# Kernel optimization log

Measured on AMD Instinct MI355X. Metric: run time of the kernel, lower is better.

Reference implementation:

```python
import jax, jax.numpy as jnp
import numpy as np

ROI = 268          # nodes per graph / input feature dim
G = 512            # graphs in batch
N = G * ROI        # total nodes = 137216
E = 1000000        # total edges
CH = 32            # GIN hidden channels
SLOPE = 0.33       # leaky relu negative slope
BN_EPS = 1e-5


def _leaky(h):
    return jnp.where(h > 0, h, SLOPE * h)


def _bn(h, g, b, m, v):
    # inference-mode batch norm with running stats
    return (h - m) * jax.lax.rsqrt(v + BN_EPS) * g + b


def _gin(x, src, dst, eps, W1, b1, W2, b2, g, b, m, v):
    # GINConv: mlp((1+eps)*x + sum_{j->i} x_j), then BN + LeakyReLU
    agg = jax.ops.segment_sum(x[src], dst, num_segments=x.shape[0])
    h = (1.0 + eps) * x + agg
    h = _leaky(h @ W1 + b1) @ W2 + b2
    return _leaky(_bn(h, g, b, m, v))


def _pool(x, batch, counts):
    mx = jax.ops.segment_max(x, batch, num_segments=G)
    mn = jax.ops.segment_sum(x, batch, num_segments=G) / counts[:, None]
    return jnp.concatenate([mx, mn], axis=-1)


def setup_inputs() -> dict:
    key = jax.random.key(0)
    ks = jax.random.split(key, 16)
    x = jax.random.normal(ks[0], (N, ROI), dtype=jnp.float32)
    # edges constrained within each graph: node = graph_id*ROI + local_idx
    gid = jax.random.randint(ks[1], (E,), 0, G, dtype=jnp.int32)
    src = gid * ROI + jax.random.randint(ks[2], (E,), 0, ROI, dtype=jnp.int32)
    dst = gid * ROI + jax.random.randint(ks[3], (E,), 0, ROI, dtype=jnp.int32)
    edge_index = jnp.stack([src, dst], axis=0)
    batch = jnp.repeat(jnp.arange(G, dtype=jnp.int32), ROI)

    def lin(k, fi, fo):
        return jax.random.normal(k, (fi, fo), dtype=jnp.float32) / np.sqrt(fi)

    kp = jax.random.split(ks[4], 16)
    inp = {
        'x': x, 'edge_index': edge_index, 'batch': batch,
        # GIN layer 0 (268 -> 32)
        'eps0': jnp.zeros((), jnp.float32),
        'W1_0': lin(kp[0], ROI, CH), 'b1_0': jnp.zeros((CH,), jnp.float32),
        'W2_0': lin(kp[1], CH, CH), 'b2_0': jnp.zeros((CH,), jnp.float32),
        'bn0_g': jnp.ones((CH,), jnp.float32), 'bn0_b': jnp.zeros((CH,), jnp.float32),
        'bn0_m': jnp.zeros((CH,), jnp.float32), 'bn0_v': jnp.ones((CH,), jnp.float32),
        # GIN layer 1 (32 -> 32)
        'eps1': jnp.zeros((), jnp.float32),
        'W1_1': lin(kp[2], CH, CH), 'b1_1': jnp.zeros((CH,), jnp.float32),
        'W2_1': lin(kp[3], CH, CH), 'b2_1': jnp.zeros((CH,), jnp.float32),
        'bn1_g': jnp.ones((CH,), jnp.float32), 'bn1_b': jnp.zeros((CH,), jnp.float32),
        'bn1_m': jnp.zeros((CH,), jnp.float32), 'bn1_v': jnp.ones((CH,), jnp.float32),
        # readout head: 4*CH=128 -> 256 -> 128 -> 1
        'lin1_W': lin(kp[4], 4 * CH, 256), 'lin1_b': jnp.zeros((256,), jnp.float32),
        'hbn1_g': jnp.ones((256,), jnp.float32), 'hbn1_b': jnp.zeros((256,), jnp.float32),
        'hbn1_m': jnp.zeros((256,), jnp.float32), 'hbn1_v': jnp.ones((256,), jnp.float32),
        'lin2_W': lin(kp[5], 256, 128), 'lin2_b': jnp.zeros((128,), jnp.float32),
        'hbn2_g': jnp.ones((128,), jnp.float32), 'hbn2_b': jnp.zeros((128,), jnp.float32),
        'hbn2_m': jnp.zeros((128,), jnp.float32), 'hbn2_v': jnp.ones((128,), jnp.float32),
        'lin3_W': lin(kp[6], 128, 1), 'lin3_b': jnp.zeros((1,), jnp.float32),
    }
    return inp


def reference(x, edge_index, batch,
              eps0, W1_0, b1_0, W2_0, b2_0, bn0_g, bn0_b, bn0_m, bn0_v,
              eps1, W1_1, b1_1, W2_1, b2_1, bn1_g, bn1_b, bn1_m, bn1_v,
              lin1_W, lin1_b, hbn1_g, hbn1_b, hbn1_m, hbn1_v,
              lin2_W, lin2_b, hbn2_g, hbn2_b, hbn2_m, hbn2_v,
              lin3_W, lin3_b):
    src, dst = edge_index[0], edge_index[1]
    counts = jax.ops.segment_sum(jnp.ones((x.shape[0],), x.dtype), batch, num_segments=G)
    h0 = _gin(x, src, dst, eps0, W1_0, b1_0, W2_0, b2_0, bn0_g, bn0_b, bn0_m, bn0_v)
    p0 = _pool(h0, batch, counts)                      # [G, 2*CH]
    h1 = _gin(h0, src, dst, eps1, W1_1, b1_1, W2_1, b2_1, bn1_g, bn1_b, bn1_m, bn1_v)
    p1 = _pool(h1, batch, counts)                      # [G, 2*CH]
    z = jnp.concatenate([p0, p1], axis=-1)             # [G, 4*CH]
    z = _leaky(_bn(z @ lin1_W + lin1_b, hbn1_g, hbn1_b, hbn1_m, hbn1_v))
    z = _leaky(_bn(z @ lin2_W + lin2_b, hbn2_g, hbn2_b, hbn2_m, hbn2_v))
    return z @ lin3_W + lin3_b                          # [G, 1]
```

## Files before the change

kernel.cpp:

```cpp
#include <hip/hip_runtime.h>

#define ROI 268
#define NG 512
#define NNODES (NG * ROI)
#define CH 32
#define SLOPE 0.33f
#define BN_EPS 1e-5f
#define SR 34
#define SAS 258
#define RPS (ROI + 1)

__device__ __forceinline__ float leakyf(float v) {
    return v > 0.f ? v : SLOPE * v;
}

__global__ __launch_bounds__(256)
__attribute__((amdgpu_waves_per_eu(2, 4))) void k_gemm1(
    const float* __restrict__ x, const float* __restrict__ W1,
    float* __restrict__ y0) {
    __shared__ float sW[ROI * CH];
    __shared__ float sA[32 * SAS];

    const int tid = threadIdx.x;
    const int l = tid & 63;
    const int wcb = __builtin_amdgcn_readfirstlane((tid >> 6) << 3);
    const size_t rowbase = (size_t)blockIdx.x * 256;

    float acc[4][8];
#pragma unroll
    for (int r = 0; r < 4; r++)
#pragma unroll
        for (int c = 0; c < 8; c++) acc[r][c] = 0.f;

#pragma unroll
    for (int i = 0; i < 9; i++) {
        int f = (i << 8) + tid;
        if (f < (ROI * CH) / 4) ((float4*)sW)[f] = ((const float4*)W1)[f];
    }

    float4 pf[8];
#pragma unroll
    for (int i = 0; i < 8; i++) {
        int f = (i << 8) + tid;
        int row = f >> 3, kc = (f & 7) << 2;
        pf[i] = *(const float4*)&x[(rowbase + row) * ROI + kc];
    }

    int k0 = 0;
    for (int chunk = 0; chunk < 9; ++chunk) {
        const int ksize = (chunk < 8) ? 32 : 12;
        if (ksize == 32) {
#pragma unroll
            for (int i = 0; i < 8; i++) {
                int f = (i << 8) + tid;
                int row = f >> 3, kc = (f & 7) << 2;
                sA[(kc + 0) * SAS + row] = pf[i].x;
                sA[(kc + 1) * SAS + row] = pf[i].y;
                sA[(kc + 2) * SAS + row] = pf[i].z;
                sA[(kc + 3) * SAS + row] = pf[i].w;
            }
        } else {
#pragma unroll
            for (int i = 0; i < 3; i++) {
                int kc = i << 2;
                sA[(kc + 0) * SAS + tid] = pf[i].x;
                sA[(kc + 1) * SAS + tid] = pf[i].y;
                sA[(kc + 2) * SAS + tid] = pf[i].z;
                sA[(kc + 3) * SAS + tid] = pf[i].w;
            }
        }
        __syncthreads();
        if (chunk + 1 < 9) {
            const int nk0 = k0 + ksize;
            if (chunk + 1 < 8) {
#pragma unroll
                for (int i = 0; i < 8; i++) {
                    int f = (i << 8) + tid;
                    int row = f >> 3, kc = (f & 7) << 2;
                    pf[i] = *(const float4*)&x[(rowbase + row) * ROI + nk0 + kc];
                }
            } else {
#pragma unroll
                for (int i = 0; i < 3; i++)
                    pf[i] = *(const float4*)&x[(rowbase + tid) * ROI + nk0 + (i << 2)];
            }
        }
        const float* wp = &sW[k0 * CH + wcb];
#pragma unroll 2
        for (int kk = 0; kk < ksize; ++kk) {
            float2 a0 = *(const float2*)&sA[kk * SAS + 2 * l];
            float2 a1 = *(const float2*)&sA[kk * SAS + 128 + 2 * l];
            float4 w0 = *(const float4*)&wp[kk * CH];
            float4 w1 = *(const float4*)&wp[kk * CH + 4];
            float av[4] = {a0.x, a0.y, a1.x, a1.y};
            float wv[8] = {w0.x, w0.y, w0.z, w0.w, w1.x, w1.y, w1.z, w1.w};
#pragma unroll
            for (int r = 0; r < 4; r++)
#pragma unroll
                for (int c = 0; c < 8; c++) acc[r][c] += av[r] * wv[c];
        }
        k0 += ksize;
        __syncthreads();
    }

#pragma unroll
    for (int r = 0; r < 4; r++) {
        size_t row = rowbase + ((r < 2) ? (2 * l + r) : (126 + 2 * l + r));
        *(float4*)&y0[row * CH + wcb] =
            make_float4(acc[r][0], acc[r][1], acc[r][2], acc[r][3]);
        *(float4*)&y0[row * CH + wcb + 4] =
            make_float4(acc[r][4], acc[r][5], acc[r][6], acc[r][7]);
    }
}

__global__ void k_deg(const int* __restrict__ dst, int E, int* __restrict__ deg) {
    int stride = gridDim.x * blockDim.x;
    for (int i = blockIdx.x * blockDim.x + threadIdx.x; i < E; i += stride)
        atomicAdd(&deg[dst[i]], 1);
}

__global__ __launch_bounds__(512) void k_scan_local(
    int* __restrict__ deg, int* __restrict__ ticket, int* __restrict__ row_ptr) {
    __shared__ int s[512];
    __shared__ int sbase;
    const int g = blockIdx.x, t = threadIdx.x;
    int v = (t < ROI) ? deg[g * ROI + t] : 0;
    s[t] = v;
    __syncthreads();
    for (int d = 1; d < 512; d <<= 1) {
        int u = (t >= d) ? s[t - d] : 0;
        __syncthreads();
        s[t] += u;
        __syncthreads();
    }
    if (t == 511) sbase = atomicAdd(ticket, s[511]);
    __syncthreads();
    const int base = sbase;
    if (t < ROI) {
        int exc = base + s[t] - v;
        row_ptr[g * RPS + t] = exc;
        deg[g * ROI + t] = exc;
    }
    if (t == 511) row_ptr[g * RPS + ROI] = base + s[511];
}

__global__ void k_fill(const int* __restrict__ src, const int* __restrict__ dst,
                       int E, int* __restrict__ rcur, int* __restrict__ ebuf) {
    int stride = gridDim.x * blockDim.x;
    for (int i = blockIdx.x * blockDim.x + threadIdx.x; i < E; i += stride) {
        int d = dst[i];
        int g = d / ROI;
        int pos = atomicAdd(&rcur[d], 1);
        ebuf[pos] = (src[i] - g * ROI) * SR;
    }
}

__device__ __forceinline__ void gather_combine(
    const float* __restrict__ in, float* __restrict__ out,
    const int* __restrict__ rp, const int* __restrict__ ebuf, float e,
    const float* __restrict__ b1, int t) {
    const int ch = t & 31;
    const int hw = t >> 5;
    for (int n = hw; n < ROI; n += 16) {
        int b = rp[n], en = rp[n + 1];
        float acc = 0.f;
        int j = b;
        for (; j + 3 < en; j += 4) {
            int p0 = ebuf[j], p1 = ebuf[j + 1], p2 = ebuf[j + 2], p3 = ebuf[j + 3];
            float v0 = in[p0 + ch], v1 = in[p1 + ch];
            float v2 = in[p2 + ch], v3 = in[p3 + ch];
            acc += (v0 + v1) + (v2 + v3);
        }
        for (; j < en; ++j) acc += in[ebuf[j] + ch];
        out[n * SR + ch] = leakyf(e * in[n * SR + ch] + acc + b1[ch]);
    }
}

template <bool AFFINE>
__device__ __forceinline__ void gemm_inplace(float* __restrict__ buf,
                                             const float* __restrict__ w,
                                             const float* __restrict__ bias,
                                             const float* __restrict__ sc,
                                             const float* __restrict__ sh, int t) {
    for (int u = t; u < ROI * 2; u += 512) {
        const int r0 = (u >> 2) * 2;
        const int cq = u & 3;
        float acc0[8], acc1[8];
#pragma unroll
        for (int c = 0; c < 8; c++) {
            float b = AFFINE ? bias[cq * 8 + c] : 0.f;
            acc0[c] = b;
            acc1[c] = b;
        }
        const float* row0 = &buf[r0 * SR];
        const float* row1 = row0 + SR;
#pragma unroll 2
        for (int k = 0; k < CH; k += 2) {
            float2 a0 = *(const float2*)&row0[k];
            float2 a1 = *(const float2*)&row1[k];
            const float* wr0 = &w[k * CH + cq * 8];
            const float* wr1 = wr0 + CH;
            float4 wa = *(const float4*)wr0;
            float4 wb = *(const float4*)(wr0 + 4);
            float4 wc = *(const float4*)wr1;
            float4 wd = *(const float4*)(wr1 + 4);
            acc0[0] += a0.x * wa.x + a0.y * wc.x;
            acc0[1] += a0.x * wa.y + a0.y * wc.y;
            acc0[2] += a0.x * wa.z + a0.y * wc.z;
            acc0[3] += a0.x * wa.w + a0.y * wc.w;
            acc0[4] += a0.x * wb.x + a0.y * wd.x;
            acc0[5] += a0.x * wb.y + a0.y * wd.y;
            acc0[6] += a0.x * wb.z + a0.y * wd.z;
            acc0[7] += a0.x * wb.w + a0.y * wd.w;
            acc1[0] += a1.x * wa.x + a1.y * wc.x;
            acc1[1] += a1.x * wa.y + a1.y * wc.y;
            acc1[2] += a1.x * wa.z + a1.y * wc.z;
            acc1[3] += a1.x * wa.w + a1.y * wc.w;
            acc1[4] += a1.x * wb.x + a1.y * wd.x;
            acc1[5] += a1.x * wb.y + a1.y * wd.y;
            acc1[6] += a1.x * wb.z + a1.y * wd.z;
            acc1[7] += a1.x * wb.w + a1.y * wd.w;
        }
        float* o0 = &buf[r0 * SR + cq * 8];
        float* o1 = o0 + SR;
#pragma unroll
        for (int c = 0; c < 8; c += 2) {
            float h00 = acc0[c], h01 = acc0[c + 1];
            float h10 = acc1[c], h11 = acc1[c + 1];
            if (AFFINE) {
                float s0 = sc[cq * 8 + c], t0 = sh[cq * 8 + c];
                float s1 = sc[cq * 8 + c + 1], t1 = sh[cq * 8 + c + 1];
                h00 = leakyf(h00 * s0 + t0);
                h01 = leakyf(h01 * s1 + t1);
                h10 = leakyf(h10 * s0 + t0);
                h11 = leakyf(h11 * s1 + t1);
            }
            *(float2*)&o0[c] = make_float2(h00, h01);
            *(float2*)&o1[c] = make_float2(h10, h11);
        }
    }
}

__device__ __forceinline__ void pool_store(const float* __restrict__ h,
                                           float* __restrict__ psc, int t) {
    const int ch = t & 31;
    const int hw = t >> 5;
    const int wave = t >> 6;
    float s = 0.f, m = -1e30f;
    for (int n = hw; n < ROI; n += 16) {
        float v = h[n * SR + ch];
        s += v;
        m = fmaxf(m, v);
    }
    s += __shfl_down(s, 32);
    m = fmaxf(m, __shfl_down(m, 32));
    if ((t & 63) < 32) {
        psc[wave * 32 + ch] = s;
        psc[256 + wave * 32 + ch] = m;
    }
}

__device__ __forceinline__ void pool_final(const float* __restrict__ psc,
                                           float* __restrict__ zg, int t) {
    if (t < 32) {
        float s = 0.f, m = -1e30f;
#pragma unroll
        for (int wv = 0; wv < 8; wv++) {
            s += psc[wv * 32 + t];
            m = fmaxf(m, psc[256 + wv * 32 + t]);
        }
        zg[t] = m;
        zg[CH + t] = s / (float)ROI;
    }
}

__global__ __launch_bounds__(512, 2) void k_gin(
    const float* __restrict__ y0, const int* __restrict__ row_ptr,
    const int* __restrict__ ebuf, const float* __restrict__ eps0p,
    const float* __restrict__ b1_0, const float* __restrict__ W2_0,
    const float* __restrict__ b2_0, const float* __restrict__ bn0_g,
    const float* __restrict__ bn0_b, const float* __restrict__ bn0_m,
    const float* __restrict__ bn0_v, const float* __restrict__ eps1p,
    const float* __restrict__ W1_1, const float* __restrict__ b1_1,
    const float* __restrict__ W2_1, const float* __restrict__ b2_1,
    const float* __restrict__ bn1_g, const float* __restrict__ bn1_b,
    const float* __restrict__ bn1_m, const float* __restrict__ bn1_v,
    float* __restrict__ z) {
    __shared__ float bufA[ROI * SR];
    __shared__ float bufB[ROI * SR];
    __shared__ float w[CH * CH];
    __shared__ float prm[8 * CH];
    __shared__ float psc[512];
    __shared__ float epss[2];

    const int t = threadIdx.x;
    const int g = blockIdx.x;

    if (t < CH) {
        prm[0 * CH + t] = b1_0[t];
        prm[1 * CH + t] = b2_0[t];
        float s0 = bn0_g[t] * rsqrtf(bn0_v[t] + BN_EPS);
        prm[2 * CH + t] = s0;
        prm[3 * CH + t] = bn0_b[t] - bn0_m[t] * s0;
        prm[4 * CH + t] = b1_1[t];
        prm[5 * CH + t] = b2_1[t];
        float s1 = bn1_g[t] * rsqrtf(bn1_v[t] + BN_EPS);
        prm[6 * CH + t] = s1;
        prm[7 * CH + t] = bn1_b[t] - bn1_m[t] * s1;
    }
    if (t == 0) {
        epss[0] = 1.0f + *eps0p;
        epss[1] = 1.0f + *eps1p;
    }

    const float* yg = y0 + (size_t)g * ROI * CH;
    for (int f = t; f < (ROI * CH) / 4; f += 512) {
        float4 v = ((const float4*)yg)[f];
        int row = f >> 3, c4 = (f & 7) << 2;
        float* p = &bufA[row * SR + c4];
        *(float2*)p = make_float2(v.x, v.y);
        *(float2*)(p + 2) = make_float2(v.z, v.w);
    }
    for (int i = t; i < (CH * CH) / 4; i += 512)
        ((float4*)w)[i] = ((const float4*)W2_0)[i];
    __syncthreads();

    const int* rp = row_ptr + g * RPS;

    gather_combine(bufA, bufB, rp, ebuf, epss[0], &prm[0 * CH], t);
    __syncthreads();

    gemm_inplace<true>(bufB, w, &prm[1 * CH], &prm[2 * CH], &prm[3 * CH], t);
    __syncthreads();

    pool_store(bufB, psc, t);
    for (int i = t; i < (CH * CH) / 4; i += 512)
        ((float4*)w)[i] = ((const float4*)W1_1)[i];
    __syncthreads();

    pool_final(psc, z + (size_t)g * 128, t);
    gemm_inplace<false>(bufB, w, nullptr, nullptr, nullptr, t);
    __syncthreads();

    gather_combine(bufB, bufA, rp, ebuf, epss[1], &prm[4 * CH], t);
    for (int i = t; i < (CH * CH) / 4; i += 512)
        ((float4*)w)[i] = ((const float4*)W2_1)[i];
    __syncthreads();

    gemm_inplace<true>(bufA, w, &prm[5 * CH], &prm[6 * CH], &prm[7 * CH], t);
    __syncthreads();

    pool_store(bufA, psc, t);
    __syncthreads();
    pool_final(psc, z + (size_t)g * 128 + 64, t);
}

__global__ __launch_bounds__(256) void k_head(
    const float* __restrict__ z, const float* __restrict__ W1,
    const float* __restrict__ b1, const float* __restrict__ g1,
    const float* __restrict__ be1, const float* __restrict__ m1,
    const float* __restrict__ v1, const float* __restrict__ W2,
    const float* __restrict__ b2, const float* __restrict__ g2,
    const float* __restrict__ be2, const float* __restrict__ m2,
    const float* __restrict__ v2, const float* __restrict__ W3,
    const float* __restrict__ b3, float* __restrict__ out) {
    __shared__ float zr[128], z1[256], z2[128];
    const int t = threadIdx.x;
    const int g = blockIdx.x;

    if (t < 32) ((float4*)zr)[t] = ((const float4*)(z + (size_t)g * 128))[t];
    __syncthreads();
    {
        float acc = b1[t];
#pragma unroll 8
        for (int k = 0; k < 128; k++) acc += zr[k] * W1[k * 256 + t];
        float s = g1[t] * rsqrtf(v1[t] + BN_EPS);
        acc = (acc - m1[t]) * s + be1[t];
        z1[t] = leakyf(acc);
    }
    __syncthreads();
    if (t < 128) {
        float acc = b2[t];
#pragma unroll 8
        for (int k = 0; k < 256; k++) acc += z1[k] * W2[k * 128 + t];
        float s = g2[t] * rsqrtf(v2[t] + BN_EPS);
        acc = (acc - m2[t]) * s + be2[t];
        z2[t] = leakyf(acc);
    }
    __syncthreads();
    if (t < 64) {
        float v = z2[t] * W3[t] + z2[t + 64] * W3[t + 64];
        for (int offd = 32; offd; offd >>= 1) v += __shfl_down(v, offd);
        if (t == 0) out[g] = v + b3[0];
    }
}

extern "C" void kernel_launch(void* const* d_in, const int* in_sizes, int n_in,
                              void* d_out, int out_size, void* d_ws, size_t ws_size,
                              hipStream_t stream) {
    const float* x      = (const float*)d_in[0];
    const int* eidx     = (const int*)d_in[1];
    const float* eps0   = (const float*)d_in[3];
    const float* W1_0   = (const float*)d_in[4];
    const float* b1_0   = (const float*)d_in[5];
    const float* W2_0   = (const float*)d_in[6];
    const float* b2_0   = (const float*)d_in[7];
    const float* bn0_g  = (const float*)d_in[8];
    const float* bn0_b  = (const float*)d_in[9];
    const float* bn0_m  = (const float*)d_in[10];
    const float* bn0_v  = (const float*)d_in[11];
    const float* eps1   = (const float*)d_in[12];
    const float* W1_1   = (const float*)d_in[13];
    const float* b1_1   = (const float*)d_in[14];
    const float* W2_1   = (const float*)d_in[15];
    const float* b2_1   = (const float*)d_in[16];
    const float* bn1_g  = (const float*)d_in[17];
    const float* bn1_b  = (const float*)d_in[18];
    const float* bn1_m  = (const float*)d_in[19];
    const float* bn1_v  = (const float*)d_in[20];
    const float* lin1_W = (const float*)d_in[21];
    const float* lin1_b = (const float*)d_in[22];
    const float* hbn1_g = (const float*)d_in[23];
    const float* hbn1_b = (const float*)d_in[24];
    const float* hbn1_m = (const float*)d_in[25];
    const float* hbn1_v = (const float*)d_in[26];
    const float* lin2_W = (const float*)d_in[27];
    const float* lin2_b = (const float*)d_in[28];
    const float* hbn2_g = (const float*)d_in[29];
    const float* hbn2_b = (const float*)d_in[30];
    const float* hbn2_m = (const float*)d_in[31];
    const float* hbn2_v = (const float*)d_in[32];
    const float* lin3_W = (const float*)d_in[33];
    const float* lin3_b = (const float*)d_in[34];

    const int E = in_sizes[1] / 2;
    const int* src = eidx;
    const int* dst = eidx + E;

    char* ws = (char*)d_ws;
    const size_t Y0_OFF  = 0;
    const size_t Z_OFF   = (size_t)NNODES * CH * 4;
    const size_t DEG_OFF = Z_OFF + (size_t)NG * 128 * 4;
    const size_t TKT_OFF = DEG_OFF + (size_t)NNODES * 4;
    const size_t RP_OFF  = TKT_OFF + 64;
    const size_t EB_OFF  = RP_OFF + (size_t)(NG * RPS + 4) * 4;

    float* y0    = (float*)(ws + Y0_OFF);
    float* z     = (float*)(ws + Z_OFF);
    int* deg     = (int*)(ws + DEG_OFF);
    int* ticket  = (int*)(ws + TKT_OFF);
    int* row_ptr = (int*)(ws + RP_OFF);
    int* ebuf    = (int*)(ws + EB_OFF);

    k_gemm1<<<NNODES / 256, 256, 0, stream>>>(x, W1_0, y0);

    hipMemsetAsync(deg, 0, (size_t)NNODES * sizeof(int) + 64, stream);
    k_deg<<<1024, 256, 0, stream>>>(dst, E, deg);
    k_scan_local<<<NG, 512, 0, stream>>>(deg, ticket, row_ptr);
    k_fill<<<1024, 256, 0, stream>>>(src, dst, E, deg, ebuf);

    k_gin<<<NG, 512, 0, stream>>>(y0, row_ptr, ebuf, eps0, b1_0, W2_0, b2_0,
                                  bn0_g, bn0_b, bn0_m, bn0_v, eps1, W1_1, b1_1,
                                  W2_1, b2_1, bn1_g, bn1_b, bn1_m, bn1_v, z);

    k_head<<<NG, 256, 0, stream>>>(z, lin1_W, lin1_b, hbn1_g, hbn1_b, hbn1_m,
                                   hbn1_v, lin2_W, lin2_b, hbn2_g, hbn2_b,
                                   hbn2_m, hbn2_v, lin3_W, lin3_b,
                                   (float*)d_out);
}
```

Measured before the change: 507.6 us.

## Replace LDS-tiled first-layer GEMM with one-row-per-thread direct-load kernel

Drops the shared-memory tiled GEMM for x@W1, which staged transposed x chunks and W1 in LDS with register prefetch. Each thread now computes one output row, reading its x row with float4 loads and W1 straight from global memory. W1 reads are wave-uniform, so they may become scalar loads. The new version removes LDS traffic and barriers, but its x loads are strided by the row length across lanes, which hurts coalescing, and it adds register pressure from 32 accumulators.

```diff
diff --git a/kernel.cpp b/kernel.cpp
--- a/kernel.cpp
+++ b/kernel.cpp
@@ -7,110 +7,39 @@
 #define SLOPE 0.33f
 #define BN_EPS 1e-5f
 #define SR 34
-#define SAS 258
 #define RPS (ROI + 1)
 
 __device__ __forceinline__ float leakyf(float v) {
     return v > 0.f ? v : SLOPE * v;
 }
 
-__global__ __launch_bounds__(256)
-__attribute__((amdgpu_waves_per_eu(2, 4))) void k_gemm1(
+__global__ __launch_bounds__(256) void k_gemm1(
     const float* __restrict__ x, const float* __restrict__ W1,
     float* __restrict__ y0) {
-    __shared__ float sW[ROI * CH];
-    __shared__ float sA[32 * SAS];
-
-    const int tid = threadIdx.x;
-    const int l = tid & 63;
-    const int wcb = __builtin_amdgcn_readfirstlane((tid >> 6) << 3);
-    const size_t rowbase = (size_t)blockIdx.x * 256;
-
-    float acc[4][8];
-#pragma unroll
-    for (int r = 0; r < 4; r++)
-#pragma unroll
-        for (int c = 0; c < 8; c++) acc[r][c] = 0.f;
-
-#pragma unroll
-    for (int i = 0; i < 9; i++) {
-        int f = (i << 8) + tid;
-        if (f < (ROI * CH) / 4) ((float4*)sW)[f] = ((const float4*)W1)[f];
-    }
-
-    float4 pf[8];
-#pragma unroll
-    for (int i = 0; i < 8; i++) {
-        int f = (i << 8) + tid;
-        int row = f >> 3, kc = (f & 7) << 2;
-        pf[i] = *(const float4*)&x[(rowbase + row) * ROI + kc];
-    }
-
-    int k0 = 0;
-    for (int chunk = 0; chunk < 9; ++chunk) {
-        const int ksize = (chunk < 8) ? 32 : 12;
-        if (ksize == 32) {
-#pragma unroll
-            for (int i = 0; i < 8; i++) {
-                int f = (i << 8) + tid;
-                int row = f >> 3, kc = (f & 7) << 2;
-                sA[(kc + 0) * SAS + row] = pf[i].x;
-                sA[(kc + 1) * SAS + row] = pf[i].y;
-                sA[(kc + 2) * SAS + row] = pf[i].z;
-                sA[(kc + 3) * SAS + row] = pf[i].w;
-            }
-        } else {
-#pragma unroll
-            for (int i = 0; i < 3; i++) {
-                int kc = i << 2;
-                sA[(kc + 0) * SAS + tid] = pf[i].x;
-                sA[(kc + 1) * SAS + tid] = pf[i].y;
-                sA[(kc + 2) * SAS + tid] = pf[i].z;
-                sA[(kc + 3) * SAS + tid] = pf[i].w;
-            }
-        }
-        __syncthreads();
-        if (chunk + 1 < 9) {
-            const int nk0 = k0 + ksize;
-            if (chunk + 1 < 8) {
-#pragma unroll
-                for (int i = 0; i < 8; i++) {
-                    int f = (i << 8) + tid;
-                    int row = f >> 3, kc = (f & 7) << 2;
-                    pf[i] = *(const float4*)&x[(rowbase + row) * ROI + nk0 + kc];
-                }
-            } else {
-#pragma unroll
-                for (int i = 0; i < 3; i++)
-                    pf[i] = *(const float4*)&x[(rowbase + tid) * ROI + nk0 + (i << 2)];
-            }
-        }
-        const float* wp = &sW[k0 * CH + wcb];
+    const size_t row = (size_t)blockIdx.x * 256 + threadIdx.x;
+    const float* __restrict__ xr = x + row * ROI;
+
+    float acc[CH];
+#pragma unroll
+    for (int c = 0; c < CH; c++) acc[c] = 0.f;
+
 #pragma unroll 2
-        for (int kk = 0; kk < ksize; ++kk) {
-            float2 a0 = *(const float2*)&sA[kk * SAS + 2 * l];
-            float2 a1 = *(const float2*)&sA[kk * SAS + 128 + 2 * l];
-            float4 w0 = *(const float4*)&wp[kk * CH];
-            float4 w1 = *(const float4*)&wp[kk * CH + 4];
-            float av[4] = {a0.x, a0.y, a1.x, a1.y};
-            float wv[8] = {w0.x, w0.y, w0.z, w0.w, w1.x, w1.y, w1.z, w1.w};
-#pragma unroll
-            for (int r = 0; r < 4; r++)
-#pragma unroll
-                for (int c = 0; c < 8; c++) acc[r][c] += av[r] * wv[c];
-        }
-        k0 += ksize;
-        __syncthreads();
-    }
-
-#pragma unroll
-    for (int r = 0; r < 4; r++) {
-        size_t row = rowbase + ((r < 2) ? (2 * l + r) : (126 + 2 * l + r));
-        *(float4*)&y0[row * CH + wcb] =
-            make_float4(acc[r][0], acc[r][1], acc[r][2], acc[r][3]);
-        *(float4*)&y0[row * CH + wcb + 4] =
-            make_float4(acc[r][4], acc[r][5], acc[r][6], acc[r][7]);
-    }
+    for (int k4 = 0; k4 < ROI; k4 += 4) {
+        float4 a = *(const float4*)&xr[k4];
+        float av[4] = {a.x, a.y, a.z, a.w};
+#pragma unroll
+        for (int j = 0; j < 4; j++) {
+            const float* __restrict__ wr = &W1[(k4 + j) * CH];
+            const float aj = av[j];
+#pragma unroll
+            for (int c = 0; c < CH; c++) acc[c] += aj * wr[c];
+        }
+    }
+
+    float* __restrict__ yr = y0 + row * CH;
+#pragma unroll
+    for (int c = 0; c < CH; c += 4)
+        *(float4*)&yr[c] = make_float4(acc[c], acc[c + 1], acc[c + 2], acc[c + 3]);
 }
 
 __global__ void k_deg(const int* __restrict__ dst, int E, int* __restrict__ deg) {
```

New measurement: 554.7 us. 9.3% more time.
